# Optimization experiments

Measured on AMD Instinct MI355X. Metric: run time of the kernel, lower is better.

Reference implementation:

```python
import jax, jax.numpy as jnp
import numpy as np

N_SRC0, N_DST0, N_DST1 = 100000, 20000, 4000
E0, E1 = 640000, 128000
IN_F, HID_F, OUT_F = 512, 512, 256


def _graph_conv(x_src, src, dst, W, b, n_src, n_dst):
    """DGL GraphConv, norm='both': D_out^{-1/2} A D_in^{-1/2} X W + b."""
    ones_e = jnp.ones(src.shape[0], x_src.dtype)
    out_deg = jnp.maximum(jax.ops.segment_sum(ones_e, src, num_segments=n_src), 1.0)
    in_deg = jnp.maximum(jax.ops.segment_sum(ones_e, dst, num_segments=n_dst), 1.0)
    h = x_src * (out_deg ** -0.5)[:, None]          # [n_src, F] pre-normalize
    agg = jax.ops.segment_sum(h[src], dst, num_segments=n_dst)  # gather -> scatter-add
    agg = agg * (in_deg ** -0.5)[:, None]           # [n_dst, F]
    return agg @ W + b


def setup_inputs() -> dict:
    key = jax.random.key(0)
    ks = jax.random.split(key, 8)
    x = jax.random.normal(ks[0], (N_SRC0, IN_F), jnp.float32)
    src0 = jax.random.randint(ks[1], (E0,), 0, N_SRC0)
    dst0 = jax.random.randint(ks[2], (E0,), 0, N_DST0)
    src1 = jax.random.randint(ks[3], (E1,), 0, N_DST0)
    dst1 = jax.random.randint(ks[4], (E1,), 0, N_DST1)
    W1 = jax.random.normal(ks[5], (IN_F, HID_F), jnp.float32) * (IN_F ** -0.5)
    b1 = jnp.zeros((HID_F,), jnp.float32)
    W2 = jax.random.normal(ks[6], (HID_F, OUT_F), jnp.float32) * (HID_F ** -0.5)
    b2 = jnp.zeros((OUT_F,), jnp.float32)
    return {"x": x, "src0": src0, "dst0": dst0, "src1": src1, "dst1": dst1,
            "W1": W1, "b1": b1, "W2": W2, "b2": b2,
            "n_src0": N_SRC0, "n_dst0": N_DST0, "n_dst1": N_DST1}


def reference(x, src0, dst0, src1, dst1, W1, b1, W2, b2, n_src0, n_dst0, n_dst1):
    h = jax.nn.relu(_graph_conv(x, src0, dst0, W1, b1, n_src0, n_dst0))
    out = jax.nn.relu(_graph_conv(h, src1, dst1, W2, b2, n_dst0, n_dst1))
    return out
```

## Files before the change

kernel.cpp:

```cpp
#include <hip/hip_runtime.h>

typedef unsigned short ushort_t;
typedef unsigned int uint_t;
typedef __attribute__((ext_vector_type(8))) short s8v;
typedef __attribute__((ext_vector_type(4))) float f4v;

#define NS0 100000
#define ND0 20000
#define ND1 4000
#define E0  640000
#define E1  128000
#define F   512
#define OF  256

__device__ __forceinline__ ushort_t f2b(float f) {
    uint_t u = __float_as_uint(f);
    uint_t r = (u + 0x7fffu + ((u >> 16) & 1u)) >> 16;
    return (ushort_t)r;
}
__device__ __forceinline__ float b2f_lo(uint_t u) { return __uint_as_float(u << 16); }
__device__ __forceinline__ float b2f_hi(uint_t u) { return __uint_as_float(u & 0xffff0000u); }

__global__ __launch_bounds__(256) void count_deg(const int* __restrict__ src0, const int* __restrict__ dst0,
                                                 const int* __restrict__ src1, const int* __restrict__ dst1,
                                                 int* __restrict__ cnt) {
    int i = blockIdx.x * 256 + threadIdx.x;
    int stride = gridDim.x * 256;
    for (int e = i; e < E0; e += stride) {
        atomicAdd(&cnt[src0[e]], 1);
        atomicAdd(&cnt[NS0 + dst0[e]], 1);
    }
    for (int e = i; e < E1; e += stride) {
        atomicAdd(&cnt[NS0 + ND0 + src1[e]], 1);
        atomicAdd(&cnt[NS0 + ND0 + ND0 + dst1[e]], 1);
    }
}

__global__ __launch_bounds__(1024) void pre2(const int* __restrict__ cnt, float* __restrict__ rsq, int ncnt,
                                             int* __restrict__ off0, int* __restrict__ cur0,
                                             int* __restrict__ off1, int* __restrict__ cur1) {
    if (blockIdx.x >= 2) {
        int i = (blockIdx.x - 2) * 1024 + threadIdx.x;
        if (i < ncnt) rsq[i] = rsqrtf(fmaxf((float)cnt[i], 1.0f));
        return;
    }
    const int* c = blockIdx.x ? (cnt + NS0 + ND0 + ND0) : (cnt + NS0);
    int n = blockIdx.x ? ND1 : ND0;
    int* off = blockIdx.x ? off1 : off0;
    int* cur = blockIdx.x ? cur1 : cur0;
    __shared__ int wsum[16];
    __shared__ int wexc[16];
    int lid = threadIdx.x, lane = lid & 63, w = lid >> 6;
    int ch = (n + 1023) >> 10;
    int s0 = lid * ch;
    int e0 = min(s0 + ch, n);
    int sum = 0;
    for (int i = s0; i < e0; ++i) sum += c[i];
    int s = sum;
    #pragma unroll
    for (int d = 1; d < 64; d <<= 1) { int t = __shfl_up(s, d, 64); if (lane >= d) s += t; }
    if (lane == 63) wsum[w] = s;
    __syncthreads();
    if (w == 0 && lane < 16) {
        int ws = wsum[lane];
        int ss = ws;
        #pragma unroll
        for (int d = 1; d < 16; d <<= 1) { int t = __shfl_up(ss, d, 64); if (lane >= d) ss += t; }
        wexc[lane] = ss - ws;
    }
    __syncthreads();
    int run = wexc[w] + s - sum;
    for (int i = s0; i < e0; ++i) {
        int v = c[i];
        off[i] = run; cur[i] = run;
        run += v;
    }
}

__global__ __launch_bounds__(256) void fill_edges(const int* __restrict__ src0, const int* __restrict__ dst0,
                                                  const int* __restrict__ src1, const int* __restrict__ dst1,
                                                  int* __restrict__ cur0, int* __restrict__ cur1,
                                                  int* __restrict__ es0, int* __restrict__ es1) {
    int i = blockIdx.x * 256 + threadIdx.x;
    int stride = gridDim.x * 256;
    for (int e = i; e < E0; e += stride) {
        int d = dst0[e];
        int p = atomicAdd(&cur0[d], 1);
        es0[p] = src0[e];
    }
    for (int e = i; e < E1; e += stride) {
        int d = dst1[e];
        int p = atomicAdd(&cur1[d], 1);
        es1[p] = src1[e];
    }
}

#define WBLK ((F * F + F * OF) / 256)
__global__ __launch_bounds__(256) void conv_wx(const float* __restrict__ W1, const float* __restrict__ W2,
                                               ushort_t* __restrict__ wt1, ushort_t* __restrict__ wt2,
                                               const float* __restrict__ x, const float* __restrict__ rsq_out0,
                                               ushort_t* __restrict__ xb) {
    if (blockIdx.x < WBLK) {
        int i = blockIdx.x * 256 + threadIdx.x;
        if (i < F * F) {
            int k = i >> 9, n = i & (F - 1);
            wt1[n * F + k] = f2b(W1[i]);
        } else {
            int j = i - F * F;
            int k = j >> 8, n = j & (OF - 1);
            wt2[n * F + k] = f2b(W2[j]);
        }
        return;
    }
    int i = (blockIdx.x - WBLK) * 256 + threadIdx.x;
    if (i >= NS0 * 128) return;
    int row = i >> 7;
    f4v v = __builtin_nontemporal_load(((const f4v*)x) + i);
    float sc = rsq_out0[row];
    uint2 o;
    o.x = (uint_t)f2b(v.x * sc) | ((uint_t)f2b(v.y * sc) << 16);
    o.y = (uint_t)f2b(v.z * sc) | ((uint_t)f2b(v.w * sc) << 16);
    ((uint2*)xb)[i] = o;
}

__device__ __forceinline__ void add8(float* acc, uint4 u) {
    acc[0] += b2f_lo(u.x); acc[1] += b2f_hi(u.x);
    acc[2] += b2f_lo(u.y); acc[3] += b2f_hi(u.y);
    acc[4] += b2f_lo(u.z); acc[5] += b2f_hi(u.z);
    acc[6] += b2f_lo(u.w); acc[7] += b2f_hi(u.w);
}

__global__ __launch_bounds__(256) void agg_bf16(const ushort_t* __restrict__ X, const int* __restrict__ es,
                                                const int* __restrict__ off, const int* __restrict__ cnt,
                                                const float* __restrict__ rsq_in, ushort_t* __restrict__ out,
                                                int ndst) {
    int d = __builtin_amdgcn_readfirstlane(blockIdx.x * 4 + (threadIdx.x >> 6));
    if (d >= ndst) return;
    int lane = threadIdx.x & 63;
    int base = off[d], n = cnt[d];
    const uint4* Xv = (const uint4*)X;
    float acc[8] = {0.f, 0.f, 0.f, 0.f, 0.f, 0.f, 0.f, 0.f};
    int i = 0;
    for (; i + 16 <= n; i += 16) {
        uint4 u[16];
        #pragma unroll
        for (int j = 0; j < 16; ++j) u[j] = Xv[(size_t)es[base + i + j] * 64 + lane];
        #pragma unroll
        for (int j = 0; j < 16; ++j) add8(acc, u[j]);
    }
    for (; i + 4 <= n; i += 4) {
        uint4 u[4];
        #pragma unroll
        for (int j = 0; j < 4; ++j) u[j] = Xv[(size_t)es[base + i + j] * 64 + lane];
        #pragma unroll
        for (int j = 0; j < 4; ++j) add8(acc, u[j]);
    }
    for (; i < n; ++i) add8(acc, Xv[(size_t)es[base + i] * 64 + lane]);
    float sc = rsq_in[d];
    uint4 o;
    o.x = (uint_t)f2b(acc[0] * sc) | ((uint_t)f2b(acc[1] * sc) << 16);
    o.y = (uint_t)f2b(acc[2] * sc) | ((uint_t)f2b(acc[3] * sc) << 16);
    o.z = (uint_t)f2b(acc[4] * sc) | ((uint_t)f2b(acc[5] * sc) << 16);
    o.w = (uint_t)f2b(acc[6] * sc) | ((uint_t)f2b(acc[7] * sc) << 16);
    ((uint4*)out)[(size_t)d * 64 + lane] = o;
}

__global__ __launch_bounds__(256) void agg_f32(const float* __restrict__ X, const float* __restrict__ rsq_out,
                                               const int* __restrict__ es, const int* __restrict__ off,
                                               const int* __restrict__ cnt, const float* __restrict__ rsq_in,
                                               ushort_t* __restrict__ out) {
    int d = blockIdx.x;
    int t = threadIdx.x;
    int base = off[d], n = cnt[d];
    float ax = 0.f, ay = 0.f;
    for (int i = 0; i < n; ++i) {
        int s = es[base + i];
        float2 v = ((const float2*)X)[(size_t)s * 256 + t];
        float sc = rsq_out[s];
        ax += v.x * sc;
        ay += v.y * sc;
    }
    float sc = rsq_in[d];
    ax *= sc; ay *= sc;
    ((uint_t*)out)[(size_t)d * 256 + t] = (uint_t)f2b(ax) | ((uint_t)f2b(ay) << 16);
}

template <typename OutT>
__global__ __launch_bounds__(256) void gemm128(const ushort_t* __restrict__ A, const ushort_t* __restrict__ BT,
                                               const float* __restrict__ bias, const float* __restrict__ rowScale,
                                               OutT* __restrict__ C, int M, int N, int K) {
    __shared__ __align__(16) ushort_t As[128 * 64];
    __shared__ __align__(16) ushort_t Bs[128 * 64];
    int tid = threadIdx.x;
    int lane = tid & 63, w = tid >> 6;
    int m16 = lane & 15, quad = lane >> 4;
    int wm = w & 1, wn = w >> 1;
    int bm = blockIdx.x * 128, bn = blockIdx.y * 128;
    f4v acc[4][4] = {};
    for (int k0 = 0; k0 < K; k0 += 64) {
        #pragma unroll
        for (int i = 0; i < 4; ++i) {
            int c = i * 256 + tid;
            int row = c >> 3, seg = (c & 7) * 8;
            int ra = bm + row; if (ra >= M) ra = M - 1;
            __builtin_amdgcn_global_load_lds(
                (const __attribute__((address_space(1))) uint_t*)(A + (size_t)ra * K + k0 + seg),
                (__attribute__((address_space(3))) uint_t*)(As + (size_t)c * 8), 16, 0, 0);
        }
        #pragma unroll
        for (int i = 0; i < 4; ++i) {
            int c = i * 256 + tid;
            int row = c >> 3, seg = (c & 7) * 8;
            int rb = bn + row;
            __builtin_amdgcn_global_load_lds(
                (const __attribute__((address_space(1))) uint_t*)(BT + (size_t)rb * K + k0 + seg),
                (__attribute__((address_space(3))) uint_t*)(Bs + (size_t)c * 8), 16, 0, 0);
        }
        __syncthreads();
        #pragma unroll
        for (int kc = 0; kc < 2; ++kc) {
            int co = kc * 32 + quad * 8;
            s8v af[4], bf[4];
            #pragma unroll
            for (int m = 0; m < 4; ++m)
                af[m] = *(const s8v*)&As[(wm * 64 + m * 16 + m16) * 64 + co];
            #pragma unroll
            for (int nn = 0; nn < 4; ++nn)
                bf[nn] = *(const s8v*)&Bs[(wn * 64 + nn * 16 + m16) * 64 + co];
            #pragma unroll
            for (int m = 0; m < 4; ++m)
                #pragma unroll
                for (int nn = 0; nn < 4; ++nn)
                    acc[m][nn] = __builtin_amdgcn_mfma_f32_16x16x32_bf16(af[m], bf[nn], acc[m][nn], 0, 0, 0);
        }
        __syncthreads();
    }
    #pragma unroll
    for (int m = 0; m < 4; ++m) {
        #pragma unroll
        for (int rr = 0; rr < 4; ++rr) {
            int row = bm + wm * 64 + m * 16 + quad * 4 + rr;
            if (row < M) {
                float rs = rowScale ? rowScale[row] : 1.0f;
                #pragma unroll
                for (int nn = 0; nn < 4; ++nn) {
                    int col = bn + wn * 64 + nn * 16 + m16;
                    float v = fmaxf(acc[m][nn][rr] + bias[col], 0.0f) * rs;
                    if (sizeof(OutT) == 2)
                        ((ushort_t*)C)[(size_t)row * N + col] = f2b(v);
                    else
                        ((float*)C)[(size_t)row * N + col] = v;
                }
            }
        }
    }
}

extern "C" void kernel_launch(void* const* d_in, const int* in_sizes, int n_in,
                              void* d_out, int out_size, void* d_ws, size_t ws_size,
                              hipStream_t stream) {
    (void)in_sizes; (void)n_in; (void)out_size;
    const float* x    = (const float*)d_in[0];
    const int*   src0 = (const int*)d_in[1];
    const int*   dst0 = (const int*)d_in[2];
    const int*   src1 = (const int*)d_in[3];
    const int*   dst1 = (const int*)d_in[4];
    const float* W1   = (const float*)d_in[5];
    const float* b1   = (const float*)d_in[6];
    const float* W2   = (const float*)d_in[7];
    const float* b2   = (const float*)d_in[8];
    float* out = (float*)d_out;

    char* p = (char*)d_ws;
    auto alloc = [&](size_t bytes) { char* q = p; p += (bytes + 255) & ~(size_t)255; return q; };
    const int NCNT = NS0 + ND0 + ND0 + ND1;
    int*      cnt  = (int*)alloc((size_t)NCNT * 4);
    float*    rsq  = (float*)alloc((size_t)NCNT * 4);
    int*      off0 = (int*)alloc((size_t)ND0 * 4);
    int*      cur0 = (int*)alloc((size_t)ND0 * 4);
    int*      off1 = (int*)alloc((size_t)ND1 * 4);
    int*      cur1 = (int*)alloc((size_t)ND1 * 4);
    int*      es0  = (int*)alloc((size_t)E0 * 4);
    int*      es1  = (int*)alloc((size_t)E1 * 4);
    ushort_t* wt1  = (ushort_t*)alloc((size_t)F * F * 2);
    ushort_t* wt2  = (ushort_t*)alloc((size_t)OF * F * 2);
    ushort_t* agg0 = (ushort_t*)alloc((size_t)ND0 * F * 2);
    ushort_t* h    = (ushort_t*)alloc((size_t)ND0 * F * 2);
    ushort_t* agg1 = (ushort_t*)alloc((size_t)ND1 * F * 2);
    size_t used = (size_t)(p - (char*)d_ws);
    bool use_xb = (ws_size >= used + (size_t)NS0 * F * 2 + 512);
    ushort_t* xb = use_xb ? (ushort_t*)alloc((size_t)NS0 * F * 2) : nullptr;

    const float* rsq_out0 = rsq;
    const float* rsq_in0  = rsq + NS0;
    const float* rsq_out1 = rsq + NS0 + ND0;
    const float* rsq_in1  = rsq + NS0 + ND0 + ND0;

    (void)hipMemsetAsync(cnt, 0, (size_t)NCNT * 4, stream);
    count_deg<<<E0 / 256, 256, 0, stream>>>(src0, dst0, src1, dst1, cnt);
    pre2<<<2 + (NCNT + 1023) / 1024, 1024, 0, stream>>>(cnt, rsq, NCNT, off0, cur0, off1, cur1);
    fill_edges<<<E0 / 256, 256, 0, stream>>>(src0, dst0, src1, dst1, cur0, cur1, es0, es1);

    if (use_xb) {
        conv_wx<<<WBLK + (NS0 * 128 + 255) / 256, 256, 0, stream>>>(W1, W2, wt1, wt2, x, rsq_out0, xb);
        agg_bf16<<<(ND0 + 3) / 4, 256, 0, stream>>>(xb, es0, off0, cnt + NS0, rsq_in0, agg0, ND0);
    } else {
        conv_wx<<<WBLK, 256, 0, stream>>>(W1, W2, wt1, wt2, x, rsq_out0, nullptr);
        agg_f32<<<ND0, 256, 0, stream>>>(x, rsq_out0, es0, off0, cnt + NS0, rsq_in0, agg0);
    }

    gemm128<ushort_t><<<dim3((ND0 + 127) / 128, F / 128), 256, 0, stream>>>(
        agg0, wt1, b1, rsq_out1, h, ND0, F, F);

    agg_bf16<<<(ND1 + 3) / 4, 256, 0, stream>>>(h, es1, off1, cnt + NS0 + ND0 + ND0, rsq_in1, agg1, ND1);

    gemm128<float><<<dim3((ND1 + 127) / 128, OF / 128), 256, 0, stream>>>(
        agg1, wt2, b2, nullptr, out, ND1, OF, F);
}
```

Measured before the change: 587.6 us.

## Gather fp32 features directly instead of pre-converting x to bf16

Drops the pass that scaled and converted all of x to bf16 in workspace, so the weight conversion becomes its own small kernel. Adds a wave-per-destination fp32 gather kernel that applies the source-degree scale per edge while accumulating. This removes a full read and write of the large input matrix. In exchange, each gathered row is twice as many bytes and the per-source scale is loaded for every edge, so the random-gather traffic doubles and relies more on cache reuse.

```diff
diff --git a/kernel.cpp b/kernel.cpp
--- a/kernel.cpp
+++ b/kernel.cpp
@@ -95,32 +95,64 @@
     }
 }
 
-#define WBLK ((F * F + F * OF) / 256)
-__global__ __launch_bounds__(256) void conv_wx(const float* __restrict__ W1, const float* __restrict__ W2,
-                                               ushort_t* __restrict__ wt1, ushort_t* __restrict__ wt2,
-                                               const float* __restrict__ x, const float* __restrict__ rsq_out0,
-                                               ushort_t* __restrict__ xb) {
-    if (blockIdx.x < WBLK) {
-        int i = blockIdx.x * 256 + threadIdx.x;
-        if (i < F * F) {
-            int k = i >> 9, n = i & (F - 1);
-            wt1[n * F + k] = f2b(W1[i]);
-        } else {
-            int j = i - F * F;
-            int k = j >> 8, n = j & (OF - 1);
-            wt2[n * F + k] = f2b(W2[j]);
-        }
-        return;
-    }
-    int i = (blockIdx.x - WBLK) * 256 + threadIdx.x;
-    if (i >= NS0 * 128) return;
-    int row = i >> 7;
-    f4v v = __builtin_nontemporal_load(((const f4v*)x) + i);
-    float sc = rsq_out0[row];
-    uint2 o;
-    o.x = (uint_t)f2b(v.x * sc) | ((uint_t)f2b(v.y * sc) << 16);
-    o.y = (uint_t)f2b(v.z * sc) | ((uint_t)f2b(v.w * sc) << 16);
-    ((uint2*)xb)[i] = o;
+__global__ __launch_bounds__(256) void conv_w(const float* __restrict__ W1, const float* __restrict__ W2,
+                                              ushort_t* __restrict__ wt1, ushort_t* __restrict__ wt2) {
+    int i = blockIdx.x * 256 + threadIdx.x;
+    if (i < F * F) {
+        int k = i >> 9, n = i & (F - 1);
+        wt1[n * F + k] = f2b(W1[i]);
+    } else if (i < F * F + F * OF) {
+        int j = i - F * F;
+        int k = j >> 8, n = j & (OF - 1);
+        wt2[n * F + k] = f2b(W2[j]);
+    }
+}
+
+__global__ __launch_bounds__(256) void agg_x_f32(const float* __restrict__ X, const float* __restrict__ rsq_out,
+                                                 const int* __restrict__ es, const int* __restrict__ off,
+                                                 const int* __restrict__ cnt, const float* __restrict__ rsq_in,
+                                                 ushort_t* __restrict__ out, int ndst) {
+    int d = __builtin_amdgcn_readfirstlane(blockIdx.x * 4 + (threadIdx.x >> 6));
+    if (d >= ndst) return;
+    int lane = threadIdx.x & 63;
+    int base = off[d], n = cnt[d];
+    const f4v* Xv = (const f4v*)X;
+    float acc[8] = {0.f, 0.f, 0.f, 0.f, 0.f, 0.f, 0.f, 0.f};
+    int i = 0;
+    for (; i + 8 <= n; i += 8) {
+        int sv[8]; float scv[8];
+        #pragma unroll
+        for (int j = 0; j < 8; ++j) { sv[j] = es[base + i + j]; scv[j] = rsq_out[sv[j]]; }
+        f4v u[16];
+        #pragma unroll
+        for (int j = 0; j < 8; ++j) {
+            u[2 * j]     = Xv[(size_t)sv[j] * 128 + lane * 2];
+            u[2 * j + 1] = Xv[(size_t)sv[j] * 128 + lane * 2 + 1];
+        }
+        #pragma unroll
+        for (int j = 0; j < 8; ++j) {
+            float sc = scv[j];
+            acc[0] += u[2*j].x * sc;   acc[1] += u[2*j].y * sc;
+            acc[2] += u[2*j].z * sc;   acc[3] += u[2*j].w * sc;
+            acc[4] += u[2*j+1].x * sc; acc[5] += u[2*j+1].y * sc;
+            acc[6] += u[2*j+1].z * sc; acc[7] += u[2*j+1].w * sc;
+        }
+    }
+    for (; i < n; ++i) {
+        int s = es[base + i];
+        float sc = rsq_out[s];
+        f4v a = Xv[(size_t)s * 128 + lane * 2];
+        f4v b = Xv[(size_t)s * 128 + lane * 2 + 1];
+        acc[0] += a.x * sc; acc[1] += a.y * sc; acc[2] += a.z * sc; acc[3] += a.w * sc;
+        acc[4] += b.x * sc; acc[5] += b.y * sc; acc[6] += b.z * sc; acc[7] += b.w * sc;
+    }
+    float sc = rsq_in[d];
+    uint4 o;
+    o.x = (uint_t)f2b(acc[0] * sc) | ((uint_t)f2b(acc[1] * sc) << 16);
+    o.y = (uint_t)f2b(acc[2] * sc) | ((uint_t)f2b(acc[3] * sc) << 16);
+    o.z = (uint_t)f2b(acc[4] * sc) | ((uint_t)f2b(acc[5] * sc) << 16);
+    o.w = (uint_t)f2b(acc[6] * sc) | ((uint_t)f2b(acc[7] * sc) << 16);
+    ((uint4*)out)[(size_t)d * 64 + lane] = o;
 }
 
 __device__ __forceinline__ void add8(float* acc, uint4 u) {
@@ -163,26 +195,6 @@
     o.z = (uint_t)f2b(acc[4] * sc) | ((uint_t)f2b(acc[5] * sc) << 16);
     o.w = (uint_t)f2b(acc[6] * sc) | ((uint_t)f2b(acc[7] * sc) << 16);
     ((uint4*)out)[(size_t)d * 64 + lane] = o;
-}
-
-__global__ __launch_bounds__(256) void agg_f32(const float* __restrict__ X, const float* __restrict__ rsq_out,
-                                               const int* __restrict__ es, const int* __restrict__ off,
-                                               const int* __restrict__ cnt, const float* __restrict__ rsq_in,
-                                               ushort_t* __restrict__ out) {
-    int d = blockIdx.x;
-    int t = threadIdx.x;
-    int base = off[d], n = cnt[d];
-    float ax = 0.f, ay = 0.f;
-    for (int i = 0; i < n; ++i) {
-        int s = es[base + i];
-        float2 v = ((const float2*)X)[(size_t)s * 256 + t];
-        float sc = rsq_out[s];
-        ax += v.x * sc;
-        ay += v.y * sc;
-    }
-    float sc = rsq_in[d];
-    ax *= sc; ay *= sc;
-    ((uint_t*)out)[(size_t)d * 256 + t] = (uint_t)f2b(ax) | ((uint_t)f2b(ay) << 16);
 }
 
 template <typename OutT>
@@ -259,7 +271,7 @@
 extern "C" void kernel_launch(void* const* d_in, const int* in_sizes, int n_in,
                               void* d_out, int out_size, void* d_ws, size_t ws_size,
                               hipStream_t stream) {
-    (void)in_sizes; (void)n_in; (void)out_size;
+    (void)in_sizes; (void)n_in; (void)out_size; (void)ws_size;
     const float* x    = (const float*)d_in[0];
     const int*   src0 = (const int*)d_in[1];
     const int*   dst0 = (const int*)d_in[2];
@@ -287,9 +299,6 @@
     ushort_t* agg0 = (ushort_t*)alloc((size_t)ND0 * F * 2);
     ushort_t* h    = (ushort_t*)alloc((size_t)ND0 * F * 2);
     ushort_t* agg1 = (ushort_t*)alloc((size_t)ND1 * F * 2);
-    size_t used = (size_t)(p - (char*)d_ws);
-    bool use_xb = (ws_size >= used + (size_t)NS0 * F * 2 + 512);
-    ushort_t* xb = use_xb ? (ushort_t*)alloc((size_t)NS0 * F * 2) : nullptr;
 
     const float* rsq_out0 = rsq;
     const float* rsq_in0  = rsq + NS0;
@@ -300,14 +309,9 @@
     count_deg<<<E0 / 256, 256, 0, stream>>>(src0, dst0, src1, dst1, cnt);
     pre2<<<2 + (NCNT + 1023) / 1024, 1024, 0, stream>>>(cnt, rsq, NCNT, off0, cur0, off1, cur1);
     fill_edges<<<E0 / 256, 256, 0, stream>>>(src0, dst0, src1, dst1, cur0, cur1, es0, es1);
-
-    if (use_xb) {
-        conv_wx<<<WBLK + (NS0 * 128 + 255) / 256, 256, 0, stream>>>(W1, W2, wt1, wt2, x, rsq_out0, xb);
-        agg_bf16<<<(ND0 + 3) / 4, 256, 0, stream>>>(xb, es0, off0, cnt + NS0, rsq_in0, agg0, ND0);
-    } else {
-        conv_wx<<<WBLK, 256, 0, stream>>>(W1, W2, wt1, wt2, x, rsq_out0, nullptr);
-        agg_f32<<<ND0, 256, 0, stream>>>(x, rsq_out0, es0, off0, cnt + NS0, rsq_in0, agg0);
-    }
+    conv_w<<<(F * F + F * OF) / 256, 256, 0, stream>>>(W1, W2, wt1, wt2);
+
+    agg_x_f32<<<(ND0 + 3) / 4, 256, 0, stream>>>(x, rsq_out0, es0, off0, cnt + NS0, rsq_in0, agg0, ND0);
 
     gemm128<ushort_t><<<dim3((ND0 + 127) / 128, F / 128), 256, 0, stream>>>(
         agg0, wt1, b1, rsq_out1, h, ND0, F, F);
```

Result: slower. 645.1 us (+9.8%).
